# Performance work log

Measured on AMD Instinct MI355X. Metric: run time of the kernel, lower is better.

Reference implementation:

```python
import jax, jax.numpy as jnp
import numpy as np
from jax import lax

J = 3  # number of decomposition levels
SQ2 = float(1.0 / np.sqrt(2.0))


def _corr(Xp, hr, axis, Lout, stride):
    """Strided valid correlation of padded Xp with taps hr along `axis`.
    out[n] = sum_k hr[k] * Xp[n*stride + k]. Tap loop is over <=10 static taps."""
    m = hr.shape[0]
    hi = stride * (Lout - 1) + 1
    acc = hr[0] * lax.slice_in_dim(Xp, 0, hi, stride, axis)
    for k in range(1, m):
        acc = acc + hr[k] * lax.slice_in_dim(Xp, k, k + hi, stride, axis)
    return acc


def colfilter(X, h):
    # 'same' convolution along H with symmetric (edge-repeat) extension.
    m = h.shape[0]; m2 = m // 2; L = X.shape[2]
    Xp = jnp.pad(X, ((0, 0), (0, 0), (m2, m2), (0, 0)), mode='symmetric')
    return _corr(Xp, h[::-1], 2, L, 1)  # corr with reversed taps == convolution


def rowfilter(X, h):
    m = h.shape[0]; m2 = m // 2; L = X.shape[3]
    Xp = jnp.pad(X, ((0, 0), (0, 0), (0, 0), (m2, m2)), mode='symmetric')
    return _corr(Xp, h[::-1], 3, L, 1)


def coldfilt(X, ha, hb, highpass):
    # Dual-tree decimated (by 2) filtering along H. r must be a multiple of 4.
    b, c, r, w = X.shape
    m = ha.shape[0]; r4 = r // 4
    Xp = jnp.pad(X, ((0, 0), (0, 0), (m, m), (0, 0)), mode='symmetric')
    E = Xp[:, :, 2::2, :]  # even-phase stream, len r/2+m-1
    O = Xp[:, :, 3::2, :]  # odd-phase stream
    a_out = _corr(O, ha[::-1], 2, r4, 2)
    b_out = _corr(E, hb[::-1], 2, r4, 2)
    ev, od = (b_out, a_out) if highpass else (a_out, b_out)
    return jnp.stack([ev, od], axis=3).reshape(b, c, r // 2, w)


def rowdfilt(X, ha, hb, highpass):
    b, c, r, w = X.shape
    m = ha.shape[0]; w4 = w // 4
    Xp = jnp.pad(X, ((0, 0), (0, 0), (0, 0), (m, m)), mode='symmetric')
    E = Xp[:, :, :, 2::2]
    O = Xp[:, :, :, 3::2]
    a_out = _corr(O, ha[::-1], 3, w4, 2)
    b_out = _corr(E, hb[::-1], 3, w4, 2)
    ev, od = (b_out, a_out) if highpass else (a_out, b_out)
    return jnp.stack([ev, od], axis=4).reshape(b, c, r, w // 2)


def q2c(y):
    # Convert quads of real pixels into two complex subbands.
    y = y * SQ2
    a = y[..., 0::2, 0::2]; b = y[..., 0::2, 1::2]
    c = y[..., 1::2, 0::2]; d = y[..., 1::2, 1::2]
    return (a - d, b + c), (a + d, b - c)


def _bands(lh, hh, hl):
    # Orientation order [15, 45, 75, 105, 135, 165] deg; real/imag in last dim.
    (r15, i15), (r165, i165) = q2c(lh)
    (r45, i45), (r135, i135) = q2c(hh)
    (r75, i75), (r105, i105) = q2c(hl)
    c = lambda re, im: jnp.stack([re, im], axis=-1)
    return jnp.stack([c(r15, i15), c(r45, i45), c(r75, i75),
                      c(r105, i105), c(r135, i135), c(r165, i165)], axis=2)


def dtcwt_forward(x, h0o, h1o, h0a, h0b, h1a, h1b):
    # Level 1 (undecimated biorthogonal filters; q2c decimates bandpass by 2).
    lo = rowfilter(x, h0o)
    hi = rowfilter(x, h1o)
    ll = colfilter(lo, h0o)
    yh = [_bands(colfilter(lo, h1o), colfilter(hi, h1o), colfilter(hi, h0o))]
    # Levels 2..J (quarter-shift dual-tree decimated filters).
    for _ in range(1, J):
        lo = rowdfilt(ll, h0b, h0a, False)
        hi = rowdfilt(ll, h1b, h1a, True)
        lh = coldfilt(lo, h1b, h1a, True)
        hl = coldfilt(hi, h0b, h0a, False)
        hh = coldfilt(hi, h1b, h1a, True)
        ll = coldfilt(lo, h0b, h0a, False)
        yh.append(_bands(lh, hh, hl))
    return (ll, yh[0], yh[1], yh[2])


def _filters():
    h0o = np.array([-0.05, 0.25, 0.6, 0.25, -0.05], dtype=np.float32)
    h1o = np.array([-3/280, 3/56, 73/280, -17/28, 73/280, 3/56, -3/280],
                   dtype=np.float32)
    h0a = np.array([0.03516384, 0.0, -0.08832942, 0.23389032, 0.76027237,
                    0.58751830, 0.0, -0.11430184, 0.0, 0.0], dtype=np.float32)
    h0b = h0a[::-1].copy()
    alt = ((-1.0) ** np.arange(10)).astype(np.float32)
    h1a = h0b * alt
    h1b = h1a[::-1].copy()
    return {k: jnp.asarray(v) for k, v in dict(
        h0o=h0o, h1o=h1o, h0a=h0a, h0b=h0b, h1a=h1a, h1b=h1b).items()}


def setup_inputs() -> dict:
    key = jax.random.key(0)
    x = jax.random.normal(key, (8, 16, 256, 256), dtype=jnp.float32)
    inp = {'x': x}
    inp.update(_filters())
    return inp


def reference(x, h0o, h1o, h0a, h0b, h1a, h1b):
    return dtcwt_forward(x, h0o, h1o, h0a, h0b, h1a, h1b)
```

## Files before the change

### kernel.cpp

```cpp
#include <hip/hip_runtime.h>

#define SQ2F 0.70710678118654752440f

static constexpr float H0O[5] = {-0.05f, 0.25f, 0.6f, 0.25f, -0.05f};
static constexpr float H1O[7] = {(float)(-3.0/280.0), (float)(3.0/56.0), (float)(73.0/280.0),
                                 (float)(-17.0/28.0), (float)(73.0/280.0), (float)(3.0/56.0),
                                 (float)(-3.0/280.0)};
static constexpr float H0A[10] = {0.03516384f, 0.0f, -0.08832942f, 0.23389032f, 0.76027237f,
                                  0.5875183f, 0.0f, -0.11430184f, 0.0f, 0.0f};
static constexpr float H0B[10] = {0.0f, 0.0f, -0.11430184f, 0.0f, 0.5875183f,
                                  0.76027237f, 0.23389032f, -0.08832942f, 0.0f, 0.03516384f};
static constexpr float H1A[10] = {0.0f, 0.0f, -0.11430184f, 0.0f, 0.5875183f,
                                  -0.76027237f, 0.23389032f, 0.08832942f, 0.0f, -0.03516384f};
static constexpr float H1B[10] = {-0.03516384f, 0.0f, 0.08832942f, 0.23389032f, -0.76027237f,
                                  0.5875183f, 0.0f, -0.11430184f, 0.0f, 0.0f};

__device__ __forceinline__ int symref(int t, int L) {
    if (t < 0) t = -1 - t;
    if (t >= L) t = 2 * L - 1 - t;
    return t;
}

__global__ __launch_bounds__(256) void level1_lds(
    const float* __restrict__ x,
    float* __restrict__ ll,
    float* __restrict__ yh0)
{
    const int H = 256, W = 256, H2 = 128, W2 = 128;
    __shared__ float Xs[38][39];
    __shared__ float Lo[38][33];
    __shared__ float Hi[38][33];

    int tid = threadIdx.x;
    int bx  = blockIdx.x;
    int tj = bx & 7, ti = (bx >> 3) & 7, bc = bx >> 6;
    int i0 = ti * 16, j0 = tj * 16;
    int gr0 = 2 * i0 - 3, gc0 = 2 * j0 - 3;
    const float* xb = x + (size_t)bc * H * W;

    for (int p = tid; p < 38 * 38; p += 256) {
        int r = p / 38, c = p - r * 38;
        Xs[r][c] = xb[(size_t)symref(gr0 + r, H) * W + symref(gc0 + c, W)];
    }
    __syncthreads();

    for (int p = tid; p < 38 * 32; p += 256) {
        int c = p / 38, r = p - c * 38;
        float l = 0.f, h = 0.f;
        #pragma unroll
        for (int t = 0; t < 5; t++) l += H0O[t] * Xs[r][c + 5 - t];
        #pragma unroll
        for (int t = 0; t < 7; t++) h += H1O[t] * Xs[r][c + 6 - t];
        Lo[r][c] = l;
        Hi[r][c] = h;
    }
    __syncthreads();

    int lj = tid & 15, li = tid >> 4;
    int i = i0 + li, j = j0 + lj;

    float lo0[8], lo1[8], hi0[8], hi1[8];
    #pragma unroll
    for (int rr = 0; rr < 8; rr++) {
        lo0[rr] = Lo[2 * li + rr][2 * lj];
        lo1[rr] = Lo[2 * li + rr][2 * lj + 1];
        hi0[rr] = Hi[2 * li + rr][2 * lj];
        hi1[rr] = Hi[2 * li + rr][2 * lj + 1];
    }

    float ll00=0,ll01=0,ll10=0,ll11=0, hl00=0,hl01=0,hl10=0,hl11=0;
    #pragma unroll
    for (int t = 0; t < 5; t++) {
        ll00 += H0O[t]*lo0[5-t]; ll01 += H0O[t]*lo1[5-t];
        ll10 += H0O[t]*lo0[6-t]; ll11 += H0O[t]*lo1[6-t];
        hl00 += H0O[t]*hi0[5-t]; hl01 += H0O[t]*hi1[5-t];
        hl10 += H0O[t]*hi0[6-t]; hl11 += H0O[t]*hi1[6-t];
    }
    float lh00=0,lh01=0,lh10=0,lh11=0, hh00=0,hh01=0,hh10=0,hh11=0;
    #pragma unroll
    for (int t = 0; t < 7; t++) {
        lh00 += H1O[t]*lo0[6-t]; lh01 += H1O[t]*lo1[6-t];
        lh10 += H1O[t]*lo0[7-t]; lh11 += H1O[t]*lo1[7-t];
        hh00 += H1O[t]*hi0[6-t]; hh01 += H1O[t]*hi1[6-t];
        hh10 += H1O[t]*hi0[7-t]; hh11 += H1O[t]*hi1[7-t];
    }

    float* llb = ll + (size_t)bc * H * W;
    llb[(size_t)(2*i)*W   + 2*j]     = ll00;
    llb[(size_t)(2*i)*W   + 2*j + 1] = ll01;
    llb[(size_t)(2*i+1)*W + 2*j]     = ll10;
    llb[(size_t)(2*i+1)*W + 2*j + 1] = ll11;

    float* yb = yh0 + (size_t)bc * 6 * H2 * W2 * 2;
    size_t pix = ((size_t)i * W2 + j) * 2;
    size_t bs  = (size_t)H2 * W2 * 2;
    {
        float a = SQ2F*lh00, b = SQ2F*lh01, c = SQ2F*lh10, d = SQ2F*lh11;
        yb[0*bs + pix] = a - d; yb[0*bs + pix + 1] = b + c;
        yb[5*bs + pix] = a + d; yb[5*bs + pix + 1] = b - c;
    }
    {
        float a = SQ2F*hh00, b = SQ2F*hh01, c = SQ2F*hh10, d = SQ2F*hh11;
        yb[1*bs + pix] = a - d; yb[1*bs + pix + 1] = b + c;
        yb[4*bs + pix] = a + d; yb[4*bs + pix + 1] = b - c;
    }
    {
        float a = SQ2F*hl00, b = SQ2F*hl01, c = SQ2F*hl10, d = SQ2F*hl11;
        yb[2*bs + pix] = a - d; yb[2*bs + pix + 1] = b + c;
        yb[3*bs + pix] = a + d; yb[3*bs + pix + 1] = b - c;
    }
}

__global__ __launch_bounds__(256) void level_fused(
    const float* __restrict__ X,
    float* __restrict__ llout,
    float* __restrict__ yh,
    int R, int C, int nbi, int nbj)
{
    __shared__ float Xs[80][81];
    __shared__ float Lo[80][33];
    __shared__ float Hi[80][33];

    int tid = threadIdx.x;
    int bx  = blockIdx.x;
    int tj = bx % nbj; int ti = (bx / nbj) % nbi; int bc = bx / (nbj * nbi);
    int i0 = ti * 16, j0 = tj * 16;
    int gr0 = 4 * i0 - 8, gc0 = 4 * j0 - 8;
    const float* Xb = X + (size_t)bc * R * C;

    for (int p = tid; p < 80 * 80; p += 256) {
        int r = p / 80, c = p - r * 80;
        Xs[r][c] = Xb[(size_t)symref(gr0 + r, R) * C + symref(gc0 + c, C)];
    }
    __syncthreads();

    for (int p = tid; p < 80 * 16; p += 256) {
        int nl = p / 80, r = p - nl * 80;
        float v[20];
        #pragma unroll
        for (int k = 0; k < 20; k++) v[k] = Xs[r][4 * nl + k];
        float aLo = 0.f, bLo = 0.f, aHi = 0.f, bHi = 0.f;
        #pragma unroll
        for (int t = 0; t < 10; t++) {
            float vo = v[19 - 2 * t], ve = v[18 - 2 * t];
            aLo += H0B[t] * vo; bLo += H0A[t] * ve;
            aHi += H1B[t] * vo; bHi += H1A[t] * ve;
        }
        Lo[r][2*nl]   = aLo;
        Lo[r][2*nl+1] = bLo;
        Hi[r][2*nl]   = bHi;
        Hi[r][2*nl+1] = aHi;
    }
    __syncthreads();

    int R4 = R >> 2, Wq = C >> 2, C2 = C >> 1;
    int lj = tid & 15, li = tid >> 4;
    int i = i0 + li, j = j0 + lj;

    float ll_[2][2], lh_[2][2], hl_[2][2], hh_[2][2];
    #pragma unroll
    for (int cc = 0; cc < 2; cc++) {
        int c = 2 * lj + cc;
        float vl[20], vh[20];
        #pragma unroll
        for (int k = 0; k < 20; k++) {
            vl[k] = Lo[4 * li + k][c];
            vh[k] = Hi[4 * li + k][c];
        }
        float a_ll=0,b_ll=0,a_lh=0,b_lh=0,a_hl=0,b_hl=0,a_hh=0,b_hh=0;
        #pragma unroll
        for (int t = 0; t < 10; t++) {
            float vo_l = vl[19 - 2*t], ve_l = vl[18 - 2*t];
            float vo_h = vh[19 - 2*t], ve_h = vh[18 - 2*t];
            a_ll += H0B[t] * vo_l;  b_ll += H0A[t] * ve_l;
            a_lh += H1B[t] * vo_l;  b_lh += H1A[t] * ve_l;
            a_hl += H0B[t] * vo_h;  b_hl += H0A[t] * ve_h;
            a_hh += H1B[t] * vo_h;  b_hh += H1A[t] * ve_h;
        }
        ll_[0][cc] = a_ll; ll_[1][cc] = b_ll;
        lh_[0][cc] = b_lh; lh_[1][cc] = a_lh;
        hl_[0][cc] = a_hl; hl_[1][cc] = b_hl;
        hh_[0][cc] = b_hh; hh_[1][cc] = a_hh;
    }

    float* llb = llout + (size_t)bc * (R >> 1) * C2;
    llb[(size_t)(2*i)*C2   + 2*j]     = ll_[0][0];
    llb[(size_t)(2*i)*C2   + 2*j + 1] = ll_[0][1];
    llb[(size_t)(2*i+1)*C2 + 2*j]     = ll_[1][0];
    llb[(size_t)(2*i+1)*C2 + 2*j + 1] = ll_[1][1];

    float* yb = yh + (size_t)bc * 6 * R4 * Wq * 2;
    size_t pix = ((size_t)i * Wq + j) * 2;
    size_t bs  = (size_t)R4 * Wq * 2;
    {
        float a = SQ2F*lh_[0][0], b = SQ2F*lh_[0][1], c = SQ2F*lh_[1][0], d = SQ2F*lh_[1][1];
        yb[0*bs + pix] = a - d; yb[0*bs + pix + 1] = b + c;
        yb[5*bs + pix] = a + d; yb[5*bs + pix + 1] = b - c;
    }
    {
        float a = SQ2F*hh_[0][0], b = SQ2F*hh_[0][1], c = SQ2F*hh_[1][0], d = SQ2F*hh_[1][1];
        yb[1*bs + pix] = a - d; yb[1*bs + pix + 1] = b + c;
        yb[4*bs + pix] = a + d; yb[4*bs + pix + 1] = b - c;
    }
    {
        float a = SQ2F*hl_[0][0], b = SQ2F*hl_[0][1], c = SQ2F*hl_[1][0], d = SQ2F*hl_[1][1];
        yb[2*bs + pix] = a - d; yb[2*bs + pix + 1] = b + c;
        yb[3*bs + pix] = a + d; yb[3*bs + pix + 1] = b - c;
    }
}

extern "C" void kernel_launch(void* const* d_in, const int* in_sizes, int n_in,
                              void* d_out, int out_size, void* d_ws, size_t ws_size,
                              hipStream_t stream) {
    const float* x = (const float*)d_in[0];
    float* out = (float*)d_out;

    const int BC = 8 * 16;

    float* out_ll  = out;
    float* out_yh0 = out + 524288;
    float* out_yh1 = out + 25690112;
    float* out_yh2 = out + 31981568;

    float* wsA = (float*)d_ws;
    float* wsB = wsA + 8388608;

    level1_lds<<<BC * 8 * 8, 256, 0, stream>>>(x, wsA, out_yh0);

    level_fused<<<BC * 4 * 4, 256, 0, stream>>>(wsA, wsB, out_yh1, 256, 256, 4, 4);

    level_fused<<<BC * 2 * 2, 256, 0, stream>>>(wsB, out_ll, out_yh2, 128, 128, 2, 2);
}
```

Measured before the change: 221.6 us.

## Fuse DTCWT levels one and two into a single tiled kernel

```diff
diff --git a/kernel.cpp b/kernel.cpp
--- a/kernel.cpp
+++ b/kernel.cpp
@@ -21,93 +21,181 @@
     return t;
 }
 
-__global__ __launch_bounds__(256) void level1_lds(
+#define XS(r,c)  S[(r)*85 + (c)]
+#define LS(r,c)  S[(r)*81 + (c)]
+#define LOS(r,c) S[4420 + (r)*81 + (c)]
+#define LO2(r,c) S[4420 + (r)*33 + (c)]
+#define HI2(r,c) S[6004 + (r)*33 + (c)]
+#define HIS(r,c) S[8632 + (r)*71 + (c)]
+
+__global__ __launch_bounds__(256) void dtcwt_l12(
     const float* __restrict__ x,
-    float* __restrict__ ll,
-    float* __restrict__ yh0)
+    float* __restrict__ yh0,
+    float* __restrict__ yh1,
+    float* __restrict__ ll2)
 {
-    const int H = 256, W = 256, H2 = 128, W2 = 128;
-    __shared__ float Xs[38][39];
-    __shared__ float Lo[38][33];
-    __shared__ float Hi[38][33];
-
-    int tid = threadIdx.x;
-    int bx  = blockIdx.x;
-    int tj = bx & 7, ti = (bx >> 3) & 7, bc = bx >> 6;
-    int i0 = ti * 16, j0 = tj * 16;
-    int gr0 = 2 * i0 - 3, gc0 = 2 * j0 - 3;
-    const float* xb = x + (size_t)bc * H * W;
-
-    for (int p = tid; p < 38 * 38; p += 256) {
-        int r = p / 38, c = p - r * 38;
-        Xs[r][c] = xb[(size_t)symref(gr0 + r, H) * W + symref(gc0 + c, W)];
-    }
-    __syncthreads();
-
-    for (int p = tid; p < 38 * 32; p += 256) {
-        int c = p / 38, r = p - c * 38;
-        float l = 0.f, h = 0.f;
-        #pragma unroll
-        for (int t = 0; t < 5; t++) l += H0O[t] * Xs[r][c + 5 - t];
-        #pragma unroll
-        for (int t = 0; t < 7; t++) h += H1O[t] * Xs[r][c + 6 - t];
-        Lo[r][c] = l;
-        Hi[r][c] = h;
-    }
-    __syncthreads();
-
-    int lj = tid & 15, li = tid >> 4;
-    int i = i0 + li, j = j0 + lj;
-
-    float lo0[8], lo1[8], hi0[8], hi1[8];
-    #pragma unroll
-    for (int rr = 0; rr < 8; rr++) {
-        lo0[rr] = Lo[2 * li + rr][2 * lj];
-        lo1[rr] = Lo[2 * li + rr][2 * lj + 1];
-        hi0[rr] = Hi[2 * li + rr][2 * lj];
-        hi1[rr] = Hi[2 * li + rr][2 * lj + 1];
-    }
-
-    float ll00=0,ll01=0,ll10=0,ll11=0, hl00=0,hl01=0,hl10=0,hl11=0;
-    #pragma unroll
-    for (int t = 0; t < 5; t++) {
-        ll00 += H0O[t]*lo0[5-t]; ll01 += H0O[t]*lo1[5-t];
-        ll10 += H0O[t]*lo0[6-t]; ll11 += H0O[t]*lo1[6-t];
-        hl00 += H0O[t]*hi0[5-t]; hl01 += H0O[t]*hi1[5-t];
-        hl10 += H0O[t]*hi0[6-t]; hl11 += H0O[t]*hi1[6-t];
-    }
-    float lh00=0,lh01=0,lh10=0,lh11=0, hh00=0,hh01=0,hh10=0,hh11=0;
-    #pragma unroll
-    for (int t = 0; t < 7; t++) {
-        lh00 += H1O[t]*lo0[6-t]; lh01 += H1O[t]*lo1[6-t];
-        lh10 += H1O[t]*lo0[7-t]; lh11 += H1O[t]*lo1[7-t];
-        hh00 += H1O[t]*hi0[6-t]; hh01 += H1O[t]*hi1[6-t];
-        hh10 += H1O[t]*hi0[7-t]; hh11 += H1O[t]*hi1[7-t];
-    }
-
-    float* llb = ll + (size_t)bc * H * W;
-    llb[(size_t)(2*i)*W   + 2*j]     = ll00;
-    llb[(size_t)(2*i)*W   + 2*j + 1] = ll01;
-    llb[(size_t)(2*i+1)*W + 2*j]     = ll10;
-    llb[(size_t)(2*i+1)*W + 2*j + 1] = ll11;
-
-    float* yb = yh0 + (size_t)bc * 6 * H2 * W2 * 2;
-    size_t pix = ((size_t)i * W2 + j) * 2;
-    size_t bs  = (size_t)H2 * W2 * 2;
+    __shared__ float S[11472];
+    int tid = threadIdx.x, bx = blockIdx.x;
+    int tj = bx & 3, ti = (bx >> 2) & 7, bc = bx >> 5;
+    const int xr0 = 32 * ti - 10, xc0 = 64 * tj - 10;
+    const float* xb = x + (size_t)bc * 65536;
+
+    for (int p = tid; p < 52 * 84; p += 256) {
+        int r = p / 84, c = p - r * 84;
+        XS(r, c) = xb[symref(xr0 + r, 256) * 256 + symref(xc0 + c, 256)];
+    }
+    __syncthreads();
+
+    for (int p = tid; p < 4160; p += 256) {
+        int r = p % 52, c = p / 52;
+        float l = 0.f;
+        #pragma unroll
+        for (int t = 0; t < 5; t++) l += H0O[t] * XS(r, c + 4 - t);
+        LOS(r, c) = l;
+    }
+    for (int p = tid; p < 2800; p += 256) {
+        int r = p % 40, c = p / 40;
+        float h = 0.f;
+        #pragma unroll
+        for (int t = 0; t < 7; t++) h += H1O[t] * XS(7 + r, c + 10 - t);
+        HIS(r, c) = h;
+    }
+    __syncthreads();
+
+    for (int p = tid; p < 3840; p += 256) {
+        int c = p % 80, r = p / 80;
+        float v = 0.f;
+        #pragma unroll
+        for (int t = 0; t < 5; t++) v += H0O[t] * LOS(r + 4 - t, c);
+        LS(r, c) = v;
+    }
     {
-        float a = SQ2F*lh00, b = SQ2F*lh01, c = SQ2F*lh10, d = SQ2F*lh11;
-        yb[0*bs + pix] = a - d; yb[0*bs + pix + 1] = b + c;
-        yb[5*bs + pix] = a + d; yb[5*bs + pix + 1] = b - c;
-    }
-    {
-        float a = SQ2F*hh00, b = SQ2F*hh01, c = SQ2F*hh10, d = SQ2F*hh11;
-        yb[1*bs + pix] = a - d; yb[1*bs + pix + 1] = b + c;
-        yb[4*bs + pix] = a + d; yb[4*bs + pix + 1] = b - c;
-    }
-    {
-        float a = SQ2F*hl00, b = SQ2F*hl01, c = SQ2F*hl10, d = SQ2F*hl11;
-        yb[2*bs + pix] = a - d; yb[2*bs + pix + 1] = b + c;
-        yb[3*bs + pix] = a + d; yb[3*bs + pix + 1] = b - c;
+        float* yb = yh0 + (size_t)bc * 196608;
+        const size_t bs = 32768;
+        for (int q = tid; q < 512; q += 256) {
+            int oj = q & 31, oi = q >> 5;
+            int i0 = 16 * ti + oi, j0 = 32 * tj + oj;
+            float low[8][2], hiw[8][2];
+            #pragma unroll
+            for (int k = 0; k < 8; k++) {
+                low[k][0] = LOS(2 * oi + 7 + k, 2 * oj + 8);
+                low[k][1] = LOS(2 * oi + 7 + k, 2 * oj + 9);
+                hiw[k][0] = HIS(2 * oi + k,     2 * oj + 3);
+                hiw[k][1] = HIS(2 * oi + k,     2 * oj + 4);
+            }
+            float lh[2][2] = {}, hh[2][2] = {}, hl[2][2] = {};
+            #pragma unroll
+            for (int t = 0; t < 7; t++) {
+                #pragma unroll
+                for (int d = 0; d < 2; d++) {
+                    lh[d][0] += H1O[t] * low[d + 6 - t][0];
+                    lh[d][1] += H1O[t] * low[d + 6 - t][1];
+                    hh[d][0] += H1O[t] * hiw[d + 6 - t][0];
+                    hh[d][1] += H1O[t] * hiw[d + 6 - t][1];
+                }
+            }
+            #pragma unroll
+            for (int t = 0; t < 5; t++) {
+                #pragma unroll
+                for (int d = 0; d < 2; d++) {
+                    hl[d][0] += H0O[t] * hiw[d + 5 - t][0];
+                    hl[d][1] += H0O[t] * hiw[d + 5 - t][1];
+                }
+            }
+            size_t pix = ((size_t)i0 * 128 + j0) * 2;
+            {
+                float a = SQ2F*lh[0][0], b = SQ2F*lh[0][1], c = SQ2F*lh[1][0], d = SQ2F*lh[1][1];
+                *(float2*)&yb[0*bs + pix] = make_float2(a - d, b + c);
+                *(float2*)&yb[5*bs + pix] = make_float2(a + d, b - c);
+            }
+            {
+                float a = SQ2F*hh[0][0], b = SQ2F*hh[0][1], c = SQ2F*hh[1][0], d = SQ2F*hh[1][1];
+                *(float2*)&yb[1*bs + pix] = make_float2(a - d, b + c);
+                *(float2*)&yb[4*bs + pix] = make_float2(a + d, b - c);
+            }
+            {
+                float a = SQ2F*hl[0][0], b = SQ2F*hl[0][1], c = SQ2F*hl[1][0], d = SQ2F*hl[1][1];
+                *(float2*)&yb[2*bs + pix] = make_float2(a - d, b + c);
+                *(float2*)&yb[3*bs + pix] = make_float2(a + d, b - c);
+            }
+        }
+    }
+    __syncthreads();
+
+    for (int p = tid; p < 768; p += 256) {
+        int r = p % 48, nl = p / 48;
+        int gc = 64 * tj + 4 * nl - 8;
+        float v[20];
+        #pragma unroll
+        for (int k = 0; k < 20; k++)
+            v[k] = LS(r, symref(gc + k, 256) - 64 * tj + 8);
+        float aLo = 0.f, bLo = 0.f, aHi = 0.f, bHi = 0.f;
+        #pragma unroll
+        for (int t = 0; t < 10; t++) {
+            float vo = v[19 - 2 * t], ve = v[18 - 2 * t];
+            aLo += H0B[t] * vo; bLo += H0A[t] * ve;
+            aHi += H1B[t] * vo; bHi += H1A[t] * ve;
+        }
+        LO2(r, 2*nl)   = aLo;
+        LO2(r, 2*nl+1) = bLo;
+        HI2(r, 2*nl)   = bHi;
+        HI2(r, 2*nl+1) = aHi;
+    }
+    __syncthreads();
+
+    if (tid < 128) {
+        int lj = tid & 15, li = tid >> 4;
+        int i1 = 8 * ti + li, j1 = 16 * tj + lj;
+
+        float ll_[2][2], lh_[2][2], hl_[2][2], hh_[2][2];
+        #pragma unroll
+        for (int cc = 0; cc < 2; cc++) {
+            int c = 2 * lj + cc;
+            float vl[20], vh[20];
+            #pragma unroll
+            for (int k = 0; k < 20; k++) {
+                int loc = symref(32 * ti + 4 * li - 8 + k, 256) - 32 * ti + 8;
+                vl[k] = LO2(loc, c);
+                vh[k] = HI2(loc, c);
+            }
+            float a_ll=0,b_ll=0,a_lh=0,b_lh=0,a_hl=0,b_hl=0,a_hh=0,b_hh=0;
+            #pragma unroll
+            for (int t = 0; t < 10; t++) {
+                float vo_l = vl[19 - 2*t], ve_l = vl[18 - 2*t];
+                float vo_h = vh[19 - 2*t], ve_h = vh[18 - 2*t];
+                a_ll += H0B[t] * vo_l;  b_ll += H0A[t] * ve_l;
+                a_lh += H1B[t] * vo_l;  b_lh += H1A[t] * ve_l;
+                a_hl += H0B[t] * vo_h;  b_hl += H0A[t] * ve_h;
+                a_hh += H1B[t] * vo_h;  b_hh += H1A[t] * ve_h;
+            }
+            ll_[0][cc] = a_ll; ll_[1][cc] = b_ll;
+            lh_[0][cc] = b_lh; lh_[1][cc] = a_lh;
+            hl_[0][cc] = a_hl; hl_[1][cc] = b_hl;
+            hh_[0][cc] = b_hh; hh_[1][cc] = a_hh;
+        }
+
+        float* llb = ll2 + (size_t)bc * 16384;
+        *(float2*)&llb[(size_t)(2*i1)  *128 + 2*j1] = make_float2(ll_[0][0], ll_[0][1]);
+        *(float2*)&llb[(size_t)(2*i1+1)*128 + 2*j1] = make_float2(ll_[1][0], ll_[1][1]);
+
+        float* yb = yh1 + (size_t)bc * 49152;
+        size_t pix = ((size_t)i1 * 64 + j1) * 2;
+        const size_t bs = 8192;
+        {
+            float a = SQ2F*lh_[0][0], b = SQ2F*lh_[0][1], c = SQ2F*lh_[1][0], d = SQ2F*lh_[1][1];
+            *(float2*)&yb[0*bs + pix] = make_float2(a - d, b + c);
+            *(float2*)&yb[5*bs + pix] = make_float2(a + d, b - c);
+        }
+        {
+            float a = SQ2F*hh_[0][0], b = SQ2F*hh_[0][1], c = SQ2F*hh_[1][0], d = SQ2F*hh_[1][1];
+            *(float2*)&yb[1*bs + pix] = make_float2(a - d, b + c);
+            *(float2*)&yb[4*bs + pix] = make_float2(a + d, b - c);
+        }
+        {
+            float a = SQ2F*hl_[0][0], b = SQ2F*hl_[0][1], c = SQ2F*hl_[1][0], d = SQ2F*hl_[1][1];
+            *(float2*)&yb[2*bs + pix] = make_float2(a - d, b + c);
+            *(float2*)&yb[3*bs + pix] = make_float2(a + d, b - c);
+        }
     }
 }
 
@@ -222,12 +310,9 @@
     float* out_yh1 = out + 25690112;
     float* out_yh2 = out + 31981568;
 
-    float* wsA = (float*)d_ws;
-    float* wsB = wsA + 8388608;
-
-    level1_lds<<<BC * 8 * 8, 256, 0, stream>>>(x, wsA, out_yh0);
-
-    level_fused<<<BC * 4 * 4, 256, 0, stream>>>(wsA, wsB, out_yh1, 256, 256, 4, 4);
-
-    level_fused<<<BC * 2 * 2, 256, 0, stream>>>(wsB, out_ll, out_yh2, 128, 128, 2, 2);
+    float* ll2 = (float*)d_ws;
+
+    dtcwt_l12<<<BC * 32, 256, 0, stream>>>(x, out_yh0, out_yh1, ll2);
+
+    level_fused<<<BC * 4, 256, 0, stream>>>(ll2, out_ll, out_yh2, 128, 128, 2, 2);
 }
```

Measured after the change: 227.1 us. 2.5% more time.
